# Optimization experiments

Measured on AMD Instinct MI355X. Metric: run time of the kernel, lower is better.

## Reference

```python
import jax, jax.numpy as jnp
import numpy as np

LATENT = 128
STEPS = 2


def _ln(x, scale, bias, eps=1e-6):
    mu = jnp.mean(x, axis=-1, keepdims=True)
    var = jnp.mean(jnp.square(x - mu), axis=-1, keepdims=True)
    return (x - mu) * jax.lax.rsqrt(var + eps) * scale + bias


def _mlp2(x, W0, b0, W1, b1):
    x = jax.nn.relu(x @ W0 + b0)
    return jax.nn.relu(x @ W1 + b1)


def setup_inputs() -> dict:
    key = jax.random.key(0)
    ks = iter(jax.random.split(key, 64))
    N, E, Dn, De, Dg, L, S = 50000, 500000, 64, 32, 16, LATENT, STEPS
    sc = 0.02
    d = {}
    d['node_feats'] = jax.random.normal(next(ks), (N, Dn), jnp.float32)
    d['edge_feats'] = jax.random.normal(next(ks), (E, De), jnp.float32)
    d['globals_'] = jax.random.normal(next(ks), (1, Dg), jnp.float32)
    d['senders'] = jax.random.randint(next(ks), (E,), 0, N, jnp.int32)
    d['receivers'] = jax.random.randint(next(ks), (E,), 0, N, jnp.int32)
    d['emb_node_W'] = jax.random.normal(next(ks), (Dn, L), jnp.float32) * sc
    d['emb_node_b'] = jnp.zeros((L,), jnp.float32)
    d['emb_edge_W'] = jax.random.normal(next(ks), (De, L), jnp.float32) * sc
    d['emb_edge_b'] = jnp.zeros((L,), jnp.float32)
    d['emb_glob_W'] = jax.random.normal(next(ks), (Dg, L), jnp.float32) * sc
    d['emb_glob_b'] = jnp.zeros((L,), jnp.float32)
    # per-step stacked params; edge/node MLP input = 4L, global MLP input = 3L
    d['edge_W0'] = jax.random.normal(next(ks), (S, 4 * L, L), jnp.float32) * sc
    d['edge_b0'] = jnp.zeros((S, L), jnp.float32)
    d['edge_W1'] = jax.random.normal(next(ks), (S, L, L), jnp.float32) * sc
    d['edge_b1'] = jnp.zeros((S, L), jnp.float32)
    d['node_W0'] = jax.random.normal(next(ks), (S, 4 * L, L), jnp.float32) * sc
    d['node_b0'] = jnp.zeros((S, L), jnp.float32)
    d['node_W1'] = jax.random.normal(next(ks), (S, L, L), jnp.float32) * sc
    d['node_b1'] = jnp.zeros((S, L), jnp.float32)
    d['glob_W0'] = jax.random.normal(next(ks), (S, 3 * L, L), jnp.float32) * sc
    d['glob_b0'] = jnp.zeros((S, L), jnp.float32)
    d['glob_W1'] = jax.random.normal(next(ks), (S, L, L), jnp.float32) * sc
    d['glob_b1'] = jnp.zeros((S, L), jnp.float32)
    d['ln_node_s'] = jnp.ones((S, L), jnp.float32)
    d['ln_node_b'] = jnp.zeros((S, L), jnp.float32)
    d['ln_edge_s'] = jnp.ones((S, L), jnp.float32)
    d['ln_edge_b'] = jnp.zeros((S, L), jnp.float32)
    d['ln_glob_s'] = jnp.ones((S, L), jnp.float32)
    d['ln_glob_b'] = jnp.zeros((S, L), jnp.float32)
    d['dec_W'] = jax.random.normal(next(ks), (L, L), jnp.float32) * sc
    d['dec_b'] = jnp.zeros((L,), jnp.float32)
    return d


def reference(node_feats, edge_feats, globals_, senders, receivers,
              emb_node_W, emb_node_b, emb_edge_W, emb_edge_b, emb_glob_W, emb_glob_b,
              edge_W0, edge_b0, edge_W1, edge_b1,
              node_W0, node_b0, node_W1, node_b1,
              glob_W0, glob_b0, glob_W1, glob_b1,
              ln_node_s, ln_node_b, ln_edge_s, ln_edge_b, ln_glob_s, ln_glob_b,
              dec_W, dec_b):
    N, E = node_feats.shape[0], edge_feats.shape[0]
    nodes = node_feats @ emb_node_W + emb_node_b          # [N, L]
    edges = edge_feats @ emb_edge_W + emb_edge_b          # [E, L]
    glob = globals_ @ emb_glob_W + emb_glob_b             # [1, L]
    for s in range(STEPS):
        # --- edge update: concat(edges, nodes[senders], nodes[receivers], global) ---
        ge = jnp.broadcast_to(glob, (E, glob.shape[-1]))
        edge_in = jnp.concatenate([edges, nodes[senders], nodes[receivers], ge], axis=-1)
        e_new = _mlp2(edge_in, edge_W0[s], edge_b0[s], edge_W1[s], edge_b1[s])
        # --- node update: concat(nodes, sum edges by sender, sum edges by receiver, global) ---
        sent = jax.ops.segment_sum(e_new, senders, num_segments=N)
        recv = jax.ops.segment_sum(e_new, receivers, num_segments=N)
        gn = jnp.broadcast_to(glob, (N, glob.shape[-1]))
        node_in = jnp.concatenate([nodes, sent, recv, gn], axis=-1)
        n_new = _mlp2(node_in, node_W0[s], node_b0[s], node_W1[s], node_b1[s])
        # --- global update: concat(sum nodes, sum edges, global) ---
        node_agg = jnp.sum(n_new, axis=0, keepdims=True)
        edge_agg = jnp.sum(e_new, axis=0, keepdims=True)
        glob_in = jnp.concatenate([node_agg, edge_agg, glob], axis=-1)
        g_new = _mlp2(glob_in, glob_W0[s], glob_b0[s], glob_W1[s], glob_b1[s])
        # skip connections + layer norm
        nodes = _ln(n_new + nodes, ln_node_s[s], ln_node_b[s])
        edges = _ln(e_new + edges, ln_edge_s[s], ln_edge_b[s])
        glob = _ln(g_new + glob, ln_glob_s[s], ln_glob_b[s])
    globals_out = glob @ dec_W + dec_b
    return nodes, edges, globals_out
```

## Files before the change

### kernel.cpp

```cpp
#include <hip/hip_runtime.h>

#define L 128
#define NSTEPS 2
#define SCAN_B 250

typedef __attribute__((ext_vector_type(8))) short short8;
typedef __attribute__((ext_vector_type(4))) float f32x4;

static __device__ __forceinline__ unsigned short f2bf(float f) {
  unsigned int u = __float_as_uint(f);
  u += 0x7FFFu + ((u >> 16) & 1u);
  return (unsigned short)(u >> 16);
}
static __device__ __forceinline__ unsigned short f2bf_trunc(float f) {
  return (unsigned short)(__float_as_uint(f) >> 16);
}
static __device__ __forceinline__ float bf2f(unsigned short h) {
  return __uint_as_float(((unsigned int)h) << 16);
}
static __device__ __forceinline__ float bfhi(unsigned u) {
  return __uint_as_float(u & 0xFFFF0000u);
}
static __device__ __forceinline__ float bflo(unsigned u) {
  return __uint_as_float(u << 16);
}
static __device__ __forceinline__ unsigned packf(float x) {
  unsigned short h = f2bf(x);
  unsigned short l = f2bf_trunc(x - bf2f(h));
  return ((unsigned)h << 16) | l;
}
static __device__ __forceinline__ float unpackf(unsigned p) {
  return bfhi(p) + bflo(p);
}

static __device__ __forceinline__ void unpack8_hi(const unsigned* __restrict__ p, short8& ah) {
  uint4 q0 = *(const uint4*)p;
  uint4 q1 = *(const uint4*)(p + 4);
  union U { unsigned u[4]; short8 s; } A;
  A.u[0] = __builtin_amdgcn_perm(q0.y, q0.x, 0x07060302u);
  A.u[1] = __builtin_amdgcn_perm(q0.w, q0.z, 0x07060302u);
  A.u[2] = __builtin_amdgcn_perm(q1.y, q1.x, 0x07060302u);
  A.u[3] = __builtin_amdgcn_perm(q1.w, q1.z, 0x07060302u);
  ah = A.s;
}

__global__ void conv_frag_kernel(const float* __restrict__ in, unsigned short* __restrict__ out,
                                 int S) {
  int id = blockIdx.x * 256 + threadIdx.x;
  int total = S * 12 * 8192;
  if (id >= total) return;
  int chunkid = id >> 13;
  int within = id & 8191;
  int s = chunkid / 12, ks = chunkid % 12;
  int hl = within >> 12;
  int rem = within & 4095;
  int fn = rem >> 9;
  int rem2 = rem & 511;
  int g = rem2 >> 7;
  int rem3 = rem2 & 127;
  int c = rem3 >> 3;
  int j = rem3 & 7;
  int k = ks * 32 + g * 8 + j;
  int n = fn * 16 + c;
  float x = in[(size_t)s * 512 * 128 + (size_t)k * 128 + n];
  unsigned short h = f2bf(x);
  out[id] = hl ? f2bf_trunc(x - bf2f(h)) : h;
}

__global__ void conv_split_kernel(const float* __restrict__ in,
                                  unsigned short* __restrict__ hi,
                                  unsigned short* __restrict__ lo,
                                  int Ksrc, int Kkeep, int S) {
  int id = blockIdx.x * 256 + threadIdx.x;
  int nk = 128 * Kkeep;
  int total = S * nk;
  if (id >= total) return;
  int s = id / nk;
  int rem = id - s * nk;
  int n = rem / Kkeep;
  int k = rem - n * Kkeep;
  float x = in[(size_t)s * Ksrc * 128 + (size_t)k * 128 + n];
  unsigned short h = f2bf(x);
  hi[id] = h;
  lo[id] = f2bf(x - bf2f(h));
}

template<int K>
__global__ __launch_bounds__(128, 4)
void embed_reg_kernel(const float* __restrict__ feats, const float* __restrict__ W,
                      const float* __restrict__ bias,
                      float* __restrict__ outf, unsigned* __restrict__ outp,
                      unsigned short* __restrict__ outh, int M) {
  int j = threadIdx.x;
  float w[K];
#pragma unroll
  for (int k = 0; k < K; ++k) w[k] = W[k * L + j];
  float bb = bias[j];
  int ng = (M + 3) >> 2;
  for (int gi = blockIdx.x; gi < ng; gi += gridDim.x) {
    int r0 = gi * 4;
    int r[4];
#pragma unroll
    for (int ri = 0; ri < 4; ++ri) r[ri] = min(r0 + ri, M - 1);
    float acc[4] = {bb, bb, bb, bb};
#pragma unroll
    for (int k4 = 0; k4 < K; k4 += 4) {
#pragma unroll
      for (int ri = 0; ri < 4; ++ri) {
        float4 f = *(const float4*)(feats + (size_t)r[ri] * K + k4);
        acc[ri] = fmaf(f.x, w[k4], acc[ri]);
        acc[ri] = fmaf(f.y, w[k4 + 1], acc[ri]);
        acc[ri] = fmaf(f.z, w[k4 + 2], acc[ri]);
        acc[ri] = fmaf(f.w, w[k4 + 3], acc[ri]);
      }
    }
#pragma unroll
    for (int ri = 0; ri < 4; ++ri) {
      size_t o = (size_t)r[ri] * L + j;
      if (outf) outf[o] = acc[ri];
      if (outp) outp[o] = packf(acc[ri]);
      if (outh) outh[o] = f2bf(acc[ri]);
    }
  }
}

__global__ void glob_embed_fold_kernel(const float* __restrict__ gin,
                                       const float* __restrict__ W, const float* __restrict__ bias,
                                       float* __restrict__ glob,
                                       const float* __restrict__ eWg, const float* __restrict__ eb0,
                                       float* __restrict__ b0e,
                                       const float* __restrict__ nWg, const float* __restrict__ nb0,
                                       float* __restrict__ b0n,
                                       float* __restrict__ node_agg, float* __restrict__ edge_agg) {
  __shared__ float gl[128];
  int j = threadIdx.x;
  float acc = bias[j];
  for (int k = 0; k < 16; ++k) acc += gin[k] * W[k * L + j];
  glob[j] = acc;
  gl[j] = acc;
  node_agg[j] = 0.f;
  edge_agg[j] = 0.f;
  __syncthreads();
  float ae = eb0[j], an = nb0[j];
  for (int k = 0; k < 128; ++k) {
    float g = gl[k];
    ae = fmaf(g, eWg[k * L + j], ae);
    an = fmaf(g, nWg[k * L + j], an);
  }
  b0e[j] = ae;
  b0n[j] = an;
}

__global__ void hist_kernel(const int* __restrict__ senders, const int* __restrict__ receivers,
                            int* __restrict__ cnt1, int* __restrict__ cnt2, int E) {
  int e = blockIdx.x * 256 + threadIdx.x;
  if (e >= E) return;
  atomicAdd(&cnt1[senders[e]], 1);
  atomicAdd(&cnt2[receivers[e]], 1);
}

__global__ void scan_sum_kernel(const int* __restrict__ cnt, int* __restrict__ part,
                                int n, int chunk) {
  __shared__ int red[256];
  int b = blockIdx.x, t = threadIdx.x;
  int lo = b * chunk, hi = min(lo + chunk, n);
  red[t] = (lo + t < hi) ? cnt[lo + t] : 0;
  __syncthreads();
  for (int o = 128; o > 0; o >>= 1) { if (t < o) red[t] += red[t + o]; __syncthreads(); }
  if (t == 0) part[b] = red[0];
}

__global__ void scan_part_kernel(int* __restrict__ part, int nb) {
  if (threadIdx.x == 0) {
    int run = 0;
    for (int i = 0; i < nb; ++i) { int v = part[i]; part[i] = run; run += v; }
  }
}

__global__ void scan_write_kernel(const int* __restrict__ cnt, const int* __restrict__ part,
                                  int* __restrict__ rp, int n, int chunk, int E) {
  __shared__ int buf[256];
  int b = blockIdx.x, t = threadIdx.x;
  int lo = b * chunk, hi = min(lo + chunk, n);
  buf[t] = (lo + t < hi) ? cnt[lo + t] : 0;
  __syncthreads();
  if (t == 0) {
    int run = part[b];
    for (int i = 0; i < hi - lo; ++i) { rp[lo + i] = run; run += buf[i]; }
  }
  if (b == gridDim.x - 1 && t == 0) rp[n] = E;
}

__global__ void fill_kernel(const int* __restrict__ senders, const int* __restrict__ receivers,
                            const int* __restrict__ rp1, const int* __restrict__ rp2,
                            int* __restrict__ cnt1, int* __restrict__ cnt2,
                            int* __restrict__ el1, int* __restrict__ el2, int E) {
  int e = blockIdx.x * 256 + threadIdx.x;
  if (e >= E) return;
  int s = senders[e];
  int p = atomicAdd(&cnt1[s], 1);
  el1[rp1[s] + p] = e;
  int r = receivers[e];
  int q = atomicAdd(&cnt2[r], 1);
  el2[rp2[r] + q] = e;
}

__global__ __launch_bounds__(256) void gather_kernel(
    const unsigned short* __restrict__ e16,
    const int* __restrict__ rp1, const int* __restrict__ el1,
    const int* __restrict__ rp2, const int* __restrict__ el2,
    unsigned short* __restrict__ sent_h, unsigned short* __restrict__ recv_h, int N) {
  int t = threadIdx.x;
  int v = blockIdx.x * 16 + (t >> 4);
  if (v >= N) return;
  int cols = (t & 15) * 8;
  float a1[8], a2[8];
#pragma unroll
  for (int i = 0; i < 8; ++i) { a1[i] = 0.f; a2[i] = 0.f; }
  int s1 = rp1[v], n1 = rp1[v + 1] - s1;
  int s2 = rp2[v], n2 = rp2[v + 1] - s2;
  int mx = max(n1, n2);
  for (int j = 0; j < mx; ++j) {
    if (j < n1) {
      uint4 u = *(const uint4*)(e16 + (size_t)el1[s1 + j] * L + cols);
      a1[0] += bflo(u.x); a1[1] += bfhi(u.x);
      a1[2] += bflo(u.y); a1[3] += bfhi(u.y);
      a1[4] += bflo(u.z); a1[5] += bfhi(u.z);
      a1[6] += bflo(u.w); a1[7] += bfhi(u.w);
    }
    if (j < n2) {
      uint4 u = *(const uint4*)(e16 + (size_t)el2[s2 + j] * L + cols);
      a2[0] += bflo(u.x); a2[1] += bfhi(u.x);
      a2[2] += bflo(u.y); a2[3] += bfhi(u.y);
      a2[4] += bflo(u.z); a2[5] += bfhi(u.z);
      a2[6] += bflo(u.w); a2[7] += bfhi(u.w);
    }
  }
  short8 o1, o2;
#pragma unroll
  for (int i = 0; i < 8; ++i) { o1[i] = (short)f2bf(a1[i]); o2[i] = (short)f2bf(a2[i]); }
  *(short8*)(sent_h + (size_t)v * L + cols) = o1;
  *(short8*)(recv_h + (size_t)v * L + cols) = o2;
}

#define WAITVM(n) do { __builtin_amdgcn_sched_barrier(0); \
  asm volatile("s_waitcnt vmcnt(" #n ")"); \
  __builtin_amdgcn_sched_barrier(0); } while (0)

template<bool EDGE_MODE>
__global__ __launch_bounds__(256, 3)
void block_step_kernel(const float* __restrict__ xf,
                       const unsigned* __restrict__ xp,
                       const unsigned short* __restrict__ g1h,
                       const unsigned short* __restrict__ g2h,
                       const int* __restrict__ idx1, const int* __restrict__ idx2,
                       const unsigned short* __restrict__ W0c,
                       const float* __restrict__ b0eff,
                       const unsigned short* __restrict__ W1h,
                       const unsigned short* __restrict__ W1l,
                       const float* __restrict__ b1,
                       const float* __restrict__ ln_s, const float* __restrict__ ln_b,
                       float* __restrict__ agg,
                       unsigned short* __restrict__ e_out,
                       float* __restrict__ xf_out,
                       unsigned* __restrict__ xp_out,
                       unsigned short* __restrict__ xh_out,
                       int M) {
  __shared__ __align__(16) unsigned short SL[16384];

  const int t = threadIdx.x;
  const int lane = t & 63;
  const int wg = t >> 6;
  const int c = lane & 15;
  const int g = lane >> 4;
  const int m0 = blockIdx.x * 128;
  const int valid = min(M - m0, 128);
  const int wbase = wg * 32;

  int rc4[2], j1[2], j2[2];
#pragma unroll
  for (int rf = 0; rf < 2; ++rf) {
    int rl = wbase + rf * 16 + c;
    int rc = min(rl, valid - 1);
    rc4[rf] = m0 + rc;
    if (EDGE_MODE) { j1[rf] = idx1[rc4[rf]]; j2[rf] = idx2[rc4[rf]]; }
    else           { j1[rf] = rc4[rf];       j2[rf] = rc4[rf]; }
  }

  const f32x4 z4 = {0.f, 0.f, 0.f, 0.f};
  f32x4 acc[2][8];
#pragma unroll
  for (int rf = 0; rf < 2; ++rf)
#pragma unroll
    for (int fn = 0; fn < 8; ++fn) acc[rf][fn] = z4;

  const char* wsrc = (const char*)W0c + (size_t)wg * 4096 + (size_t)lane * 16;
  char* slbase = (char*)&SL[0] + (size_t)wg * 4096;
  auto gllds_chunk = [&](int ks, int buf) {
    const char* gb = wsrc + (size_t)ks * 16384;
    char* lb = slbase + buf * 16384;
#pragma unroll
    for (int i = 0; i < 4; ++i) {
      __builtin_amdgcn_global_load_lds(
          (const __attribute__((address_space(1))) unsigned int*)(gb + i * 1024),
          (__attribute__((address_space(3))) unsigned int*)(lb + i * 1024),
          16, 0, 0);
    }
  };

  auto load_frag = [&](int ks, short8* a) {
    int seg = ks >> 2, kk = ks & 3;
    if (seg == 0) {
      if (EDGE_MODE) {
#pragma unroll
        for (int rf = 0; rf < 2; ++rf) {
          const float* bp = xf + (size_t)rc4[rf] * L + g * 8 + kk * 32;
          float4 v0 = *(const float4*)bp;
          float4 v1 = *(const float4*)(bp + 4);
          a[rf][0] = (short)f2bf(v0.x); a[rf][1] = (short)f2bf(v0.y);
          a[rf][2] = (short)f2bf(v0.z); a[rf][3] = (short)f2bf(v0.w);
          a[rf][4] = (short)f2bf(v1.x); a[rf][5] = (short)f2bf(v1.y);
          a[rf][6] = (short)f2bf(v1.z); a[rf][7] = (short)f2bf(v1.w);
        }
      } else {
#pragma unroll
        for (int rf = 0; rf < 2; ++rf)
          unpack8_hi(xp + (size_t)rc4[rf] * L + g * 8 + kk * 32, a[rf]);
      }
    } else {
      const unsigned short* src = (seg == 1) ? g1h : g2h;
      const int* rsel = (seg == 1) ? j1 : j2;
#pragma unroll
      for (int rf = 0; rf < 2; ++rf)
        a[rf] = *(const short8*)(src + (size_t)rsel[rf] * L + g * 8 + kk * 32);
    }
  };

  auto mfma_phase = [&](int buf, const short8* a) {
    __builtin_amdgcn_s_setprio(1);
#pragma unroll
    for (int fn = 0; fn < 8; ++fn) {
      int off = buf * 8192 + fn * 512 + g * 128 + c * 8;
      short8 bh = *(const short8*)&SL[off];
      short8 bl = *(const short8*)&SL[off + 4096];
#pragma unroll
      for (int rf = 0; rf < 2; ++rf) {
        acc[rf][fn] = __builtin_amdgcn_mfma_f32_16x16x32_bf16(a[rf], bh, acc[rf][fn], 0, 0, 0);
        acc[rf][fn] = __builtin_amdgcn_mfma_f32_16x16x32_bf16(a[rf], bl, acc[rf][fn], 0, 0, 0);
      }
    }
    __builtin_amdgcn_s_setprio(0);
  };

  {
    short8 a[5][2];
    gllds_chunk(0, 0);
    load_frag(0, a[0]);
    load_frag(1, a[1]);
    load_frag(2, a[2]);
    load_frag(3, a[3]);
    WAITVM(16);
    __builtin_amdgcn_s_barrier();

#define STEP(ks, VMW)                                             \
    {                                                             \
      if ((ks) < 11) gllds_chunk((ks) + 1, ((ks) + 1) & 1);       \
      if ((ks) < 8) load_frag((ks) + 4, a[((ks) + 4) % 5]);       \
      mfma_phase((ks) & 1, a[(ks) % 5]);                          \
      if ((ks) < 11) {                                            \
        WAITVM(VMW);                                              \
        __builtin_amdgcn_s_barrier();                             \
      }                                                           \
    }
    STEP(0, 2) STEP(1, 2) STEP(2, 2) STEP(3, 2) STEP(4, 2)
    STEP(5, 2) STEP(6, 2) STEP(7, 2) STEP(8, 0) STEP(9, 0)
    STEP(10, 0) STEP(11, 0)
#undef STEP
  }
  __syncthreads();

  unsigned short* Hbf = SL;
#pragma unroll
  for (int fn = 0; fn < 8; ++fn) {
    int col = fn * 16 + c;
    float bb = b0eff[col];
    int unit = col >> 3;
#pragma unroll
    for (int rf = 0; rf < 2; ++rf) {
#pragma unroll
      for (int ri = 0; ri < 4; ++ri) {
        int rl = wbase + rf * 16 + g * 4 + ri;
        float x = fmaxf(acc[rf][fn][ri] + bb, 0.f);
        Hbf[rl * 128 + ((unit ^ (rl & 15)) << 3) + (col & 7)] = f2bf(x);
      }
    }
  }

  f32x4 acc2[2][8];
#pragma unroll
  for (int rf = 0; rf < 2; ++rf)
#pragma unroll
    for (int fn = 0; fn < 8; ++fn) acc2[rf][fn] = z4;
#pragma unroll
  for (int ks = 0; ks < 4; ++ks) {
    short8 ah[2];
#pragma unroll
    for (int rf = 0; rf < 2; ++rf) {
      int rl = wbase + rf * 16 + c;
      int unit = ks * 4 + g;
      ah[rf] = *(const short8*)&Hbf[rl * 128 + ((unit ^ (rl & 15)) << 3)];
    }
#pragma unroll
    for (int fn = 0; fn < 8; ++fn) {
      size_t wb = (size_t)(fn * 16 + c) * 128 + ks * 32 + g * 8;
      short8 bh = *(const short8*)(W1h + wb);
      short8 bl = *(const short8*)(W1l + wb);
#pragma unroll
      for (int rf = 0; rf < 2; ++rf) {
        acc2[rf][fn] = __builtin_amdgcn_mfma_f32_16x16x32_bf16(ah[rf], bh, acc2[rf][fn], 0, 0, 0);
        acc2[rf][fn] = __builtin_amdgcn_mfma_f32_16x16x32_bf16(ah[rf], bl, acc2[rf][fn], 0, 0, 0);
      }
    }
  }

  float colagg[8];
#pragma unroll
  for (int fn = 0; fn < 8; ++fn) colagg[fn] = 0.f;

#pragma unroll
  for (int rf = 0; rf < 2; ++rf) {
    const int rb = wbase + rf * 16 + g * 4;
    float sum[4] = {0.f, 0.f, 0.f, 0.f}, sq[4] = {0.f, 0.f, 0.f, 0.f};
    float xv[8][4];
#pragma unroll
    for (int fn = 0; fn < 8; ++fn) {
      int col = fn * 16 + c;
      float bb = b1[col];
#pragma unroll
      for (int ri = 0; ri < 4; ++ri) {
        int row = rb + ri;
        float e = fmaxf(acc2[rf][fn][ri] + bb, 0.f);
        if (row < valid) {
          if (EDGE_MODE) e_out[(size_t)(m0 + row) * L + col] = f2bf(e);
          colagg[fn] += e;
          float xprev;
          if (EDGE_MODE) xprev = xf[(size_t)(m0 + row) * L + col];
          else           xprev = unpackf(xp[(size_t)(m0 + row) * L + col]);
          float x = e + xprev;
          xv[fn][ri] = x;
          sum[ri] += x;
          sq[ri] += x * x;
        } else {
          xv[fn][ri] = 0.f;
        }
      }
    }
#pragma unroll
    for (int mask = 1; mask <= 8; mask <<= 1) {
#pragma unroll
      for (int ri = 0; ri < 4; ++ri) {
        sum[ri] += __shfl_xor(sum[ri], mask);
        sq[ri] += __shfl_xor(sq[ri], mask);
      }
    }
    float mu[4], rs[4];
#pragma unroll
    for (int ri = 0; ri < 4; ++ri) {
      mu[ri] = sum[ri] * (1.f / 128.f);
      float var = sq[ri] * (1.f / 128.f) - mu[ri] * mu[ri];
      rs[ri] = rsqrtf(var + 1e-6f);
    }
#pragma unroll
    for (int fn = 0; fn < 8; ++fn) {
      int col = fn * 16 + c;
      float lns = ln_s[col], lnb = ln_b[col];
#pragma unroll
      for (int ri = 0; ri < 4; ++ri) {
        int row = rb + ri;
        if (row < valid) {
          float y = (xv[fn][ri] - mu[ri]) * rs[ri] * lns + lnb;
          if (xf_out) xf_out[(size_t)(m0 + row) * L + col] = y;
          if (xp_out) xp_out[(size_t)(m0 + row) * L + col] = packf(y);
          if (xh_out) xh_out[(size_t)(m0 + row) * L + col] = f2bf(y);
        }
      }
    }
  }

#pragma unroll
  for (int mask = 16; mask <= 32; mask <<= 1)
#pragma unroll
    for (int fn = 0; fn < 8; ++fn) colagg[fn] += __shfl_xor(colagg[fn], mask);
  __syncthreads();
  float* F = (float*)SL;
  if (lane < 16) {
#pragma unroll
    for (int fn = 0; fn < 8; ++fn) F[wg * 128 + fn * 16 + lane] = colagg[fn];
  }
  __syncthreads();
  if (t < 128) {
    float s = 0.f;
#pragma unroll
    for (int w = 0; w < 4; ++w) s += F[w * 128 + t];
    atomicAdd(agg + t, s);
  }
}

__global__ void glob_step_kernel(float* __restrict__ glob,
                                 float* __restrict__ node_agg, float* __restrict__ edge_agg,
                                 const float* __restrict__ W0, const float* __restrict__ b0,
                                 const float* __restrict__ W1, const float* __restrict__ b1,
                                 const float* __restrict__ ln_s, const float* __restrict__ ln_b,
                                 const float* __restrict__ eWg, const float* __restrict__ eb0,
                                 float* __restrict__ b0e,
                                 const float* __restrict__ nWg, const float* __restrict__ nb0,
                                 float* __restrict__ b0n) {
  __shared__ float gin[384];
  __shared__ float h[128];
  __shared__ float red4[4];
  __shared__ float gl[128];
  int j = threadIdx.x;
  gin[j] = node_agg[j];
  gin[128 + j] = edge_agg[j];
  gin[256 + j] = glob[j];
  __syncthreads();
  node_agg[j] = 0.f;
  edge_agg[j] = 0.f;
  float a = b0[j];
  for (int k = 0; k < 384; ++k) a += gin[k] * W0[k * L + j];
  h[j] = fmaxf(a, 0.f);
  __syncthreads();
  float o = b1[j];
  for (int k = 0; k < 128; ++k) o += h[k] * W1[k * L + j];
  o = fmaxf(o, 0.f);
  float x = o + gin[256 + j];
  float sum = x, sq = x * x;
  for (int m = 1; m < 64; m <<= 1) { sum += __shfl_xor(sum, m); sq += __shfl_xor(sq, m); }
  if ((j & 63) == 0) { red4[(j >> 6) * 2] = sum; red4[(j >> 6) * 2 + 1] = sq; }
  __syncthreads();
  sum = red4[0] + red4[2]; sq = red4[1] + red4[3];
  float mu = sum * (1.f / 128.f);
  float var = sq * (1.f / 128.f) - mu * mu;
  float rsd = rsqrtf(var + 1e-6f);
  float gnew = (x - mu) * rsd * ln_s[j] + ln_b[j];
  glob[j] = gnew;
  gl[j] = gnew;
  __syncthreads();
  if (eWg) {
    float ae = eb0[j], an = nb0[j];
    for (int k = 0; k < 128; ++k) {
      float g = gl[k];
      ae = fmaf(g, eWg[k * L + j], ae);
      an = fmaf(g, nWg[k * L + j], an);
    }
    b0e[j] = ae;
    b0n[j] = an;
  }
}

__global__ void decode_kernel(const float* __restrict__ glob, const float* __restrict__ W,
                              const float* __restrict__ bias, float* __restrict__ out) {
  int j = threadIdx.x;
  float a = bias[j];
  for (int k = 0; k < 128; ++k) a += glob[k] * W[k * L + j];
  out[j] = a;
}

extern "C" void kernel_launch(void* const* d_in, const int* in_sizes, int n_in,
                              void* d_out, int out_size, void* d_ws, size_t ws_size,
                              hipStream_t stream) {
  const float* node_feats = (const float*)d_in[0];
  const float* edge_feats = (const float*)d_in[1];
  const float* globals_   = (const float*)d_in[2];
  const int*   senders    = (const int*)d_in[3];
  const int*   receivers  = (const int*)d_in[4];
  const float* emb_node_W = (const float*)d_in[5];
  const float* emb_node_b = (const float*)d_in[6];
  const float* emb_edge_W = (const float*)d_in[7];
  const float* emb_edge_b = (const float*)d_in[8];
  const float* emb_glob_W = (const float*)d_in[9];
  const float* emb_glob_b = (const float*)d_in[10];
  const float* edge_W0 = (const float*)d_in[11];
  const float* edge_b0 = (const float*)d_in[12];
  const float* edge_W1 = (const float*)d_in[13];
  const float* edge_b1 = (const float*)d_in[14];
  const float* node_W0 = (const float*)d_in[15];
  const float* node_b0 = (const float*)d_in[16];
  const float* node_W1 = (const float*)d_in[17];
  const float* node_b1 = (const float*)d_in[18];
  const float* glob_W0 = (const float*)d_in[19];
  const float* glob_b0 = (const float*)d_in[20];
  const float* glob_W1 = (const float*)d_in[21];
  const float* glob_b1 = (const float*)d_in[22];
  const float* ln_node_s = (const float*)d_in[23];
  const float* ln_node_b = (const float*)d_in[24];
  const float* ln_edge_s = (const float*)d_in[25];
  const float* ln_edge_b = (const float*)d_in[26];
  const float* ln_glob_s = (const float*)d_in[27];
  const float* ln_glob_b = (const float*)d_in[28];
  const float* dec_W = (const float*)d_in[29];
  const float* dec_b = (const float*)d_in[30];

  const int N = in_sizes[0] / 64;
  const int E = in_sizes[1] / 32;

  float* nodes = (float*)d_out;
  float* edges = nodes + (size_t)N * L;
  float* gout  = edges + (size_t)E * L;

  char* wp = (char*)d_ws;
  auto alloc = [&](size_t bytes) -> char* {
    char* p = wp;
    wp += (bytes + 255) & ~(size_t)255;
    return p;
  };
  float* glob = (float*)alloc(512);
  float* node_agg = (float*)alloc(512);
  float* edge_agg = (float*)alloc(512);
  float* b0e_eff = (float*)alloc(512);
  float* b0n_eff = (float*)alloc(512);
  unsigned short* eW0c = (unsigned short*)alloc((size_t)NSTEPS * 12 * 8192 * 2);
  unsigned short* nW0c = (unsigned short*)alloc((size_t)NSTEPS * 12 * 8192 * 2);
  unsigned short* eW1h = (unsigned short*)alloc((size_t)NSTEPS * 128 * 128 * 2);
  unsigned short* eW1l = (unsigned short*)alloc((size_t)NSTEPS * 128 * 128 * 2);
  unsigned short* nW1h = (unsigned short*)alloc((size_t)NSTEPS * 128 * 128 * 2);
  unsigned short* nW1l = (unsigned short*)alloc((size_t)NSTEPS * 128 * 128 * 2);
  unsigned* nodes_p = (unsigned*)alloc((size_t)N * L * 4);
  unsigned short* nodes_h = (unsigned short*)alloc((size_t)N * L * 2);
  unsigned short* sent_h  = (unsigned short*)alloc((size_t)N * L * 2);
  unsigned short* recv_h  = (unsigned short*)alloc((size_t)N * L * 2);
  int* rp1 = (int*)alloc((size_t)(N + 1) * 4);
  int* rp2 = (int*)alloc((size_t)(N + 1) * 4);
  int* cnt1 = (int*)alloc((size_t)N * 4);
  int* cnt2 = (int*)alloc((size_t)N * 4);
  int* el1 = (int*)alloc((size_t)E * 4);
  int* el2 = (int*)alloc((size_t)E * 4);
  int* part = (int*)alloc(SCAN_B * 4);
  unsigned short* e16 = (unsigned short*)alloc((size_t)E * L * 2);
  (void)ws_size;

  conv_frag_kernel<<<(NSTEPS * 12 * 8192 + 255) / 256, 256, 0, stream>>>(edge_W0, eW0c, NSTEPS);
  conv_frag_kernel<<<(NSTEPS * 12 * 8192 + 255) / 256, 256, 0, stream>>>(node_W0, nW0c, NSTEPS);
  conv_split_kernel<<<(NSTEPS * 128 * 128 + 255) / 256, 256, 0, stream>>>(edge_W1, eW1h, eW1l, 128, 128, NSTEPS);
  conv_split_kernel<<<(NSTEPS * 128 * 128 + 255) / 256, 256, 0, stream>>>(node_W1, nW1h, nW1l, 128, 128, NSTEPS);

  embed_reg_kernel<64><<<2048, 128, 0, stream>>>(node_feats, emb_node_W, emb_node_b,
                                                 nullptr, nodes_p, nodes_h, N);
  embed_reg_kernel<32><<<4096, 128, 0, stream>>>(edge_feats, emb_edge_W, emb_edge_b,
                                                 edges, nullptr, nullptr, E);
  glob_embed_fold_kernel<<<1, 128, 0, stream>>>(globals_, emb_glob_W, emb_glob_b, glob,
                                                edge_W0 + 384 * L, edge_b0, b0e_eff,
                                                node_W0 + 384 * L, node_b0, b0n_eff,
                                                node_agg, edge_agg);

  const int chunk = (N + SCAN_B - 1) / SCAN_B;
  hipMemsetAsync(cnt1, 0, (size_t)N * 4, stream);
  hipMemsetAsync(cnt2, 0, (size_t)N * 4, stream);
  hist_kernel<<<(E + 255) / 256, 256, 0, stream>>>(senders, receivers, cnt1, cnt2, E);
  scan_sum_kernel<<<SCAN_B, 256, 0, stream>>>(cnt1, part, N, chunk);
  scan_part_kernel<<<1, 64, 0, stream>>>(part, SCAN_B);
  scan_write_kernel<<<SCAN_B, 256, 0, stream>>>(cnt1, part, rp1, N, chunk, E);
  scan_sum_kernel<<<SCAN_B, 256, 0, stream>>>(cnt2, part, N, chunk);
  scan_part_kernel<<<1, 64, 0, stream>>>(part, SCAN_B);
  scan_write_kernel<<<SCAN_B, 256, 0, stream>>>(cnt2, part, rp2, N, chunk, E);
  hipMemsetAsync(cnt1, 0, (size_t)N * 4, stream);
  hipMemsetAsync(cnt2, 0, (size_t)N * 4, stream);
  fill_kernel<<<(E + 255) / 256, 256, 0, stream>>>(senders, receivers, rp1, rp2, cnt1, cnt2, el1, el2, E);

  const int egrid = (E + 127) / 128;
  const int ngrid = (N + 127) / 128;

  for (int s = 0; s < NSTEPS; ++s) {
    const bool last = (s == NSTEPS - 1);

    block_step_kernel<true><<<egrid, 256, 0, stream>>>(
        edges, nullptr, nodes_h, nodes_h, senders, receivers,
        eW0c + (size_t)s * 12 * 8192, b0e_eff,
        eW1h + (size_t)s * 128 * 128, eW1l + (size_t)s * 128 * 128, edge_b1 + s * L,
        ln_edge_s + s * L, ln_edge_b + s * L,
        edge_agg, e16, edges, nullptr, nullptr, E);

    gather_kernel<<<(N + 15) / 16, 256, 0, stream>>>(e16, rp1, el1, rp2, el2, sent_h, recv_h, N);

    block_step_kernel<false><<<ngrid, 256, 0, stream>>>(
        nullptr, nodes_p, sent_h, recv_h, nullptr, nullptr,
        nW0c + (size_t)s * 12 * 8192, b0n_eff,
        nW1h + (size_t)s * 128 * 128, nW1l + (size_t)s * 128 * 128, node_b1 + s * L,
        ln_node_s + s * L, ln_node_b + s * L,
        node_agg, nullptr, last ? nodes : nullptr, last ? nullptr : nodes_p,
        last ? nullptr : nodes_h, N);

    glob_step_kernel<<<1, 128, 0, stream>>>(
        glob, node_agg, edge_agg,
        glob_W0 + (size_t)s * 384 * L, glob_b0 + s * L,
        glob_W1 + (size_t)s * 128 * L, glob_b1 + s * L,
        ln_glob_s + s * L, ln_glob_b + s * L,
        last ? nullptr : (edge_W0 + (size_t)1 * 512 * L + 384 * L),
        last ? nullptr : (edge_b0 + 1 * L), b0e_eff,
        last ? nullptr : (node_W0 + (size_t)1 * 512 * L + 384 * L),
        last ? nullptr : (node_b0 + 1 * L), b0n_eff);
  }

  decode_kernel<<<1, 128, 0, stream>>>(glob, dec_W, dec_b, gout);
}
```

Measured before the change: 1.559 ms.

## Scatter edge outputs into CSR-sorted buffers so gather reads contiguously

```diff
diff --git a/kernel.cpp b/kernel.cpp
--- a/kernel.cpp
+++ b/kernel.cpp
@@ -194,21 +194,31 @@
 __global__ void fill_kernel(const int* __restrict__ senders, const int* __restrict__ receivers,
                             const int* __restrict__ rp1, const int* __restrict__ rp2,
                             int* __restrict__ cnt1, int* __restrict__ cnt2,
-                            int* __restrict__ el1, int* __restrict__ el2, int E) {
+                            int* __restrict__ pos1, int* __restrict__ pos2,
+                            int* __restrict__ el2, int E) {
   int e = blockIdx.x * 256 + threadIdx.x;
   if (e >= E) return;
   int s = senders[e];
   int p = atomicAdd(&cnt1[s], 1);
-  el1[rp1[s] + p] = e;
+  pos1[e] = rp1[s] + p;
   int r = receivers[e];
   int q = atomicAdd(&cnt2[r], 1);
-  el2[rp2[r] + q] = e;
+  int w = rp2[r] + q;
+  pos2[e] = w;
+  el2[w] = e;
+}
+
+__global__ void remap_kernel(int* __restrict__ el2, const int* __restrict__ pos1, int E) {
+  int w = blockIdx.x * 256 + threadIdx.x;
+  if (w >= E) return;
+  el2[w] = pos1[el2[w]];
 }
 
 __global__ __launch_bounds__(256) void gather_kernel(
-    const unsigned short* __restrict__ e16,
-    const int* __restrict__ rp1, const int* __restrict__ el1,
-    const int* __restrict__ rp2, const int* __restrict__ el2,
+    const unsigned short* __restrict__ e1s,
+    const unsigned short* __restrict__ e2s,
+    const int* __restrict__ el2p,
+    const int* __restrict__ rp1, const int* __restrict__ rp2,
     unsigned short* __restrict__ sent_h, unsigned short* __restrict__ recv_h, int N) {
   int t = threadIdx.x;
   int v = blockIdx.x * 16 + (t >> 4);
@@ -222,14 +232,16 @@
   int mx = max(n1, n2);
   for (int j = 0; j < mx; ++j) {
     if (j < n1) {
-      uint4 u = *(const uint4*)(e16 + (size_t)el1[s1 + j] * L + cols);
+      uint4 u = *(const uint4*)(e1s + (size_t)(s1 + j) * L + cols);
       a1[0] += bflo(u.x); a1[1] += bfhi(u.x);
       a1[2] += bflo(u.y); a1[3] += bfhi(u.y);
       a1[4] += bflo(u.z); a1[5] += bfhi(u.z);
       a1[6] += bflo(u.w); a1[7] += bfhi(u.w);
     }
     if (j < n2) {
-      uint4 u = *(const uint4*)(e16 + (size_t)el2[s2 + j] * L + cols);
+      size_t row2 = e2s ? (size_t)(s2 + j) : (size_t)el2p[s2 + j];
+      const unsigned short* src = e2s ? e2s : e1s;
+      uint4 u = *(const uint4*)(src + row2 * L + cols);
       a2[0] += bflo(u.x); a2[1] += bfhi(u.x);
       a2[2] += bflo(u.y); a2[3] += bfhi(u.y);
       a2[4] += bflo(u.z); a2[5] += bfhi(u.z);
@@ -261,7 +273,8 @@
                        const float* __restrict__ b1,
                        const float* __restrict__ ln_s, const float* __restrict__ ln_b,
                        float* __restrict__ agg,
-                       unsigned short* __restrict__ e_out,
+                       const int* __restrict__ pos1, const int* __restrict__ pos2,
+                       unsigned short* __restrict__ e1s, unsigned short* __restrict__ e2s,
                        float* __restrict__ xf_out,
                        unsigned* __restrict__ xp_out,
                        unsigned short* __restrict__ xh_out,
@@ -430,6 +443,15 @@
 #pragma unroll
   for (int rf = 0; rf < 2; ++rf) {
     const int rb = wbase + rf * 16 + g * 4;
+    int sp4[4], rp4[4];
+    if (EDGE_MODE) {
+#pragma unroll
+      for (int ri = 0; ri < 4; ++ri) {
+        int rc = min(rb + ri, valid - 1);
+        sp4[ri] = pos1[m0 + rc];
+        rp4[ri] = e2s ? pos2[m0 + rc] : 0;
+      }
+    }
     float sum[4] = {0.f, 0.f, 0.f, 0.f}, sq[4] = {0.f, 0.f, 0.f, 0.f};
     float xv[8][4];
 #pragma unroll
@@ -441,7 +463,11 @@
         int row = rb + ri;
         float e = fmaxf(acc2[rf][fn][ri] + bb, 0.f);
         if (row < valid) {
-          if (EDGE_MODE) e_out[(size_t)(m0 + row) * L + col] = f2bf(e);
+          if (EDGE_MODE) {
+            unsigned short ev = f2bf(e);
+            e1s[(size_t)sp4[ri] * L + col] = ev;
+            if (e2s) e2s[(size_t)rp4[ri] * L + col] = ev;
+          }
           colagg[fn] += e;
           float xprev;
           if (EDGE_MODE) xprev = xf[(size_t)(m0 + row) * L + col];
@@ -633,11 +659,17 @@
   int* rp2 = (int*)alloc((size_t)(N + 1) * 4);
   int* cnt1 = (int*)alloc((size_t)N * 4);
   int* cnt2 = (int*)alloc((size_t)N * 4);
-  int* el1 = (int*)alloc((size_t)E * 4);
+  int* pos1 = (int*)alloc((size_t)E * 4);
+  int* pos2 = (int*)alloc((size_t)E * 4);
   int* el2 = (int*)alloc((size_t)E * 4);
   int* part = (int*)alloc(SCAN_B * 4);
-  unsigned short* e16 = (unsigned short*)alloc((size_t)E * L * 2);
-  (void)ws_size;
+  unsigned short* e1s = (unsigned short*)alloc((size_t)E * L * 2);
+  size_t need_base = (size_t)(wp - (char*)d_ws);
+  unsigned short* e2s = (unsigned short*)alloc((size_t)E * L * 2);
+  size_t need_full = (size_t)(wp - (char*)d_ws);
+  const bool two = (ws_size >= need_full);
+  (void)need_base;
+  unsigned short* e2s_use = two ? e2s : nullptr;
 
   conv_frag_kernel<<<(NSTEPS * 12 * 8192 + 255) / 256, 256, 0, stream>>>(edge_W0, eW0c, NSTEPS);
   conv_frag_kernel<<<(NSTEPS * 12 * 8192 + 255) / 256, 256, 0, stream>>>(node_W0, nW0c, NSTEPS);
@@ -665,7 +697,10 @@
   scan_write_kernel<<<SCAN_B, 256, 0, stream>>>(cnt2, part, rp2, N, chunk, E);
   hipMemsetAsync(cnt1, 0, (size_t)N * 4, stream);
   hipMemsetAsync(cnt2, 0, (size_t)N * 4, stream);
-  fill_kernel<<<(E + 255) / 256, 256, 0, stream>>>(senders, receivers, rp1, rp2, cnt1, cnt2, el1, el2, E);
+  fill_kernel<<<(E + 255) / 256, 256, 0, stream>>>(senders, receivers, rp1, rp2, cnt1, cnt2,
+                                                   pos1, pos2, el2, E);
+  if (!two)
+    remap_kernel<<<(E + 255) / 256, 256, 0, stream>>>(el2, pos1, E);
 
   const int egrid = (E + 127) / 128;
   const int ngrid = (N + 127) / 128;
@@ -678,16 +713,18 @@
         eW0c + (size_t)s * 12 * 8192, b0e_eff,
         eW1h + (size_t)s * 128 * 128, eW1l + (size_t)s * 128 * 128, edge_b1 + s * L,
         ln_edge_s + s * L, ln_edge_b + s * L,
-        edge_agg, e16, edges, nullptr, nullptr, E);
-
-    gather_kernel<<<(N + 15) / 16, 256, 0, stream>>>(e16, rp1, el1, rp2, el2, sent_h, recv_h, N);
+        edge_agg, pos1, pos2, e1s, e2s_use, edges, nullptr, nullptr, E);
+
+    gather_kernel<<<(N + 15) / 16, 256, 0, stream>>>(e1s, e2s_use, el2, rp1, rp2,
+                                                     sent_h, recv_h, N);
 
     block_step_kernel<false><<<ngrid, 256, 0, stream>>>(
         nullptr, nodes_p, sent_h, recv_h, nullptr, nullptr,
         nW0c + (size_t)s * 12 * 8192, b0n_eff,
         nW1h + (size_t)s * 128 * 128, nW1l + (size_t)s * 128 * 128, node_b1 + s * L,
         ln_node_s + s * L, ln_node_b + s * L,
-        node_agg, nullptr, last ? nodes : nullptr, last ? nullptr : nodes_p,
+        node_agg, nullptr, nullptr, nullptr, nullptr,
+        last ? nodes : nullptr, last ? nullptr : nodes_p,
         last ? nullptr : nodes_h, N);
 
     glob_step_kernel<<<1, 128, 0, stream>>>(
```

Result: slower. 1.685 ms (+8.1%).
